# Optimization experiments

Hardware: AMD Instinct MI355X
Metric: run time of the kernel (lower is better)

## Reference

```python
import jax, jax.numpy as jnp
import numpy as np

HIDDEN = 256
BATCH = 8
N_A = 2048
N_B = 2048


def setup_inputs() -> dict:
    key = jax.random.key(0)
    ks = jax.random.split(key, 9)
    s = 1.0 / np.sqrt(HIDDEN)  # torch Linear default init scale
    return {
        "A": jax.random.normal(ks[0], (BATCH, N_A, HIDDEN), dtype=jnp.float32),
        "B": jax.random.normal(ks[1], (BATCH, N_B, HIDDEN), dtype=jnp.float32),
        "mask_B": jax.random.randint(ks[2], (BATCH, N_B), 0, 2, dtype=jnp.int32),
        "Wq": jax.random.uniform(ks[3], (HIDDEN, HIDDEN), jnp.float32, -s, s),
        "bq": jax.random.uniform(ks[4], (HIDDEN,), jnp.float32, -s, s),
        "Wk": jax.random.uniform(ks[5], (HIDDEN, HIDDEN), jnp.float32, -s, s),
        "bk": jax.random.uniform(ks[6], (HIDDEN,), jnp.float32, -s, s),
        "Wv": jax.random.uniform(ks[7], (HIDDEN, HIDDEN), jnp.float32, -s, s),
        "bv": jax.random.uniform(ks[8], (HIDDEN,), jnp.float32, -s, s),
    }


def reference(A, B, mask_B, Wq, bq, Wk, bk, Wv, bv):
    # QKV projections (torch Linear: x @ W.T + b)
    Q = A @ Wq.T + bq          # [B, N_A, H]
    K = B @ Wk.T + bk          # [B, N_B, H]
    V = B @ Wv.T + bv          # [B, N_B, H]
    scale = 1.0 / jnp.sqrt(jnp.asarray(Q.shape[-1], Q.dtype))
    scores = jnp.einsum("bnh,bmh->bnm", Q, K) * scale  # [B, N_A, N_B]
    neg_inf = jnp.finfo(scores.dtype).min
    scores = jnp.where(mask_B[:, None, :] == 0, neg_inf, scores)
    attn = jax.nn.softmax(scores, axis=-1)
    out = jnp.einsum("bnm,bmh->bnh", attn, V)          # [B, N_A, H]
    return out
```

## Files before the change

kernel.cpp:

```cpp
#include <hip/hip_runtime.h>


typedef __attribute__((ext_vector_type(8))) __bf16 bf16x8;
typedef __attribute__((ext_vector_type(4))) __bf16 bf16x4;
typedef __attribute__((ext_vector_type(4))) float f32x4;

#if __has_builtin(__builtin_amdgcn_exp2f)
#define EXP2(x) __builtin_amdgcn_exp2f(x)
#else
#define EXP2(x) exp2f(x)
#endif

#define MFMA16(a, b, c) __builtin_amdgcn_mfma_f32_16x16x32_bf16((a), (b), (c), 0, 0, 0)

typedef const __attribute__((address_space(1))) char gas_char;
typedef __attribute__((address_space(3))) char las_char;

static __device__ __forceinline__ void gload16(const void* g, void* l) {
  __builtin_amdgcn_global_load_lds((gas_char*)g, (las_char*)l, 16, 0, 0);
}

static __device__ __forceinline__ bf16x8 pack8(f32x4 a, f32x4 b) {
  bf16x8 r;
  r[0] = (__bf16)a[0]; r[1] = (__bf16)a[1]; r[2] = (__bf16)a[2]; r[3] = (__bf16)a[3];
  r[4] = (__bf16)b[0]; r[5] = (__bf16)b[1]; r[6] = (__bf16)b[2]; r[7] = (__bf16)b[3];
  return r;
}

__global__ __launch_bounds__(256) void wprep_kernel(
    const float* __restrict__ Wq, const float* __restrict__ Wk,
    const float* __restrict__ Wv, const int* __restrict__ mask,
    __bf16* __restrict__ Wb, float* __restrict__ mb) {
  const int bid = blockIdx.x;
  if (bid < 96) {
    int c = bid * 256 + threadIdx.x;
    int w_id = c >> 13;
    int j = c & 8191;
    const float* __restrict__ W = (w_id == 0) ? Wq : (w_id == 1 ? Wk : Wv);
    int n = j >> 5;
    int c5 = j & 31;
    int qtr = c5 >> 3;
    int k8 = (c5 & 7) << 3;
    const float* wp = &W[n * 256 + qtr * 64 + k8];
    f32x4 w0 = *(const f32x4*)wp;
    f32x4 w1 = *(const f32x4*)(wp + 4);
    if (w_id == 0) {
      const float cs = 0.090168440f;
      w0[0] *= cs; w0[1] *= cs; w0[2] *= cs; w0[3] *= cs;
      w1[0] *= cs; w1[1] *= cs; w1[2] *= cs; w1[3] *= cs;
    }
    int kx = k8 ^ ((n & 7) << 3);
    *(bf16x8*)&Wb[(size_t)w_id * 65536 + qtr * 16384 + n * 64 + kx] =
        pack8(w0, w1);
  } else {
    int i = (bid - 96) * 256 + threadIdx.x;
    if (i < 8 * 2048) mb[i] = (mask[i] != 0) ? 0.0f : -1.0e30f;
  }
}

__global__ __launch_bounds__(256, 2) void proj_kernel(
    const float* __restrict__ A, const float* __restrict__ Bm,
    const __bf16* __restrict__ Wb,
    const float* __restrict__ bq, const float* __restrict__ bk,
    const float* __restrict__ bv,
    __bf16* __restrict__ QF, __bf16* __restrict__ KF, __bf16* __restrict__ VF) {
  extern __shared__ char smem[];
  const int pid = blockIdx.x;
  const int proj = pid >> 8;
  const int rb = (pid & 255) << 6;
  const float* __restrict__ X = (proj == 0) ? A : Bm;
  const char* __restrict__ Wbp = (const char*)(Wb + (size_t)proj * 65536);
  const float* __restrict__ bias = (proj == 0) ? bq : (proj == 1 ? bk : bv);
  const int tid = threadIdx.x;
  const int w = tid >> 6, l = tid & 63, lo = l & 15, g = l >> 4;
  const int r0 = rb + w * 16;

  bf16x8 xf[8];
#pragma unroll
  for (int q8 = 0; q8 < 8; ++q8) {
    const float* xp = &X[(r0 + lo) * 256 + q8 * 32 + g * 8];
    xf[q8] = pack8(*(const f32x4*)xp, *(const f32x4*)(xp + 4));
  }

  f32x4 acc[16];
#pragma unroll
  for (int j = 0; j < 16; ++j) acc[j] = (f32x4){0.f, 0.f, 0.f, 0.f};

  #define STAGEW(qtr, buf)                                                    \
    {                                                                         \
      const char* gw = Wbp + (qtr)*32768 + w * 1024 + l * 16;                 \
      char* lw = smem + (buf)*32768 + w * 1024;                               \
      gload16(gw, lw);                                                        \
      gload16(gw + 4096, lw + 4096);                                          \
      gload16(gw + 8192, lw + 8192);                                          \
      gload16(gw + 12288, lw + 12288);                                        \
      gload16(gw + 16384, lw + 16384);                                        \
      gload16(gw + 20480, lw + 20480);                                        \
      gload16(gw + 24576, lw + 24576);                                        \
      gload16(gw + 28672, lw + 28672);                                        \
    }

  STAGEW(0, 0);
  __syncthreads();

  for (int qtr = 0; qtr < 4; ++qtr) {
    const int cur = qtr & 1;
    if (qtr < 3) STAGEW(qtr + 1, cur ^ 1);
    const __bf16* Wl = (const __bf16*)(smem + cur * 32768);
#pragma unroll
    for (int ks2 = 0; ks2 < 2; ++ks2) {
      bf16x8 xcur = xf[qtr * 2 + ks2];
#pragma unroll
      for (int nt = 0; nt < 16; ++nt) {
        int n = nt * 16 + lo;
        int kchunk = (ks2 * 4 + g) ^ (n & 7);
        bf16x8 wf = *(const bf16x8*)&Wl[n * 64 + kchunk * 8];
        if (proj == 2) {
          acc[nt] = MFMA16(wf, xcur, acc[nt]);
        } else {
          acc[nt] = MFMA16(xcur, wf, acc[nt]);
        }
      }
    }
    __syncthreads();
  }

  if (proj != 2) {
    const float cs = (proj == 0) ? 0.090168440f : 1.0f;
    __bf16* __restrict__ O = (proj == 0) ? QF : KF;
    const size_t rgbase = (size_t)(r0 >> 4) << 12;
#pragma unroll
    for (int nt = 0; nt < 16; ++nt) {
      int h = nt * 16 + lo;
      float bb = bias[h] * cs;
      size_t hpart = (size_t)((h >> 5) << 9) + (((h >> 3) & 3) << 7) + (h & 7);
#pragma unroll
      for (int r = 0; r < 4; ++r) {
        int R = r0 + g * 4 + r;
        O[rgbase + hpart + ((R & 15) << 3)] = (__bf16)(acc[nt][r] + bb);
      }
    }
  } else {
    const int bidx = r0 >> 11;
    const int nb = r0 & 2047;
    __bf16* __restrict__ Vo = VF + (size_t)bidx * 524288;
#pragma unroll
    for (int ht = 0; ht < 16; ++ht)
#pragma unroll
      for (int r = 0; r < 4; ++r) {
        int h = ht * 16 + g * 4 + r;
        int n = nb + lo;
        Vo[((size_t)(n >> 6) << 14) + ((h >> 4) << 10) + (((n >> 3) & 7) << 7) +
           ((h & 15) << 3) + (n & 7)] = (__bf16)(acc[ht][r] + bias[h]);
      }
  }
}

__global__ __launch_bounds__(256, 2) void attn_kernel(
    const __bf16* __restrict__ QF, const __bf16* __restrict__ KF,
    const __bf16* __restrict__ VF, const float* __restrict__ mb,
    __bf16* __restrict__ Opart, float* __restrict__ mpart,
    float* __restrict__ lpart, float* __restrict__ out,
    int chunk, int direct) {
  extern __shared__ char smem[];
  const int bid = blockIdx.x;
  const int b = bid & 7;
  const int rest = bid >> 3;
  const int qt = rest & 15;
  const int s = rest >> 4;
  const int tid = threadIdx.x;
  const int w = tid >> 6, l = tid & 63, lo = l & 15, g = l >> 4;
  const int q0 = qt * 128 + w * 32;
  const __bf16* __restrict__ Qb = QF + ((size_t)b * 2048 + q0) * 256;
  const __bf16* __restrict__ Kb = KF + (size_t)b * 2048 * 256;
  const __bf16* __restrict__ Vb = VF + (size_t)b * 524288;
  const float* __restrict__ mbb = mb + b * 2048;
  __bf16* Pw = (__bf16*)(smem + 65536) + w * 1280;
  float* mbl = (float*)(smem + 75776);

  bf16x8 qf[2][8];
#pragma unroll
  for (int u = 0; u < 2; ++u)
#pragma unroll
    for (int hs = 0; hs < 8; ++hs)
      qf[u][hs] = *(const bf16x8*)&Qb[u * 4096 + hs * 512 + l * 8];

  f32x4 oacc[2][16];
#pragma unroll
  for (int u = 0; u < 2; ++u)
#pragma unroll
    for (int i = 0; i < 16; ++i) oacc[u][i] = (f32x4){0.f, 0.f, 0.f, 0.f};
  float m[2] = {-3.0e28f, -3.0e28f}, lsum[2] = {0.f, 0.f};

  const int kv0 = s * chunk;
  const int niter = chunk >> 5;

  #define STAGE_K(kvb, buf)                                                   \
    {                                                                         \
      const char* gk = (const char*)(Kb + (size_t)(kvb) * 256) + w * 4096 +   \
                       l * 16;                                                \
      char* lk = smem + (buf)*16384 + w * 4096;                               \
      gload16(gk, lk);                                                        \
      gload16(gk + 1024, lk + 1024);                                          \
      gload16(gk + 2048, lk + 2048);                                          \
      gload16(gk + 3072, lk + 3072);                                          \
    }
  #define STAGE_V(kvb, buf)                                                   \
    {                                                                         \
      const char* gv = (const char*)(Vb + (((size_t)(kvb) >> 6) << 14) +      \
                                     (((kvb) >> 5) & 1) * 512) +              \
                       w * 8192 + l * 16;                                     \
      char* lv = smem + 32768 + (buf)*16384 + w * 4096;                       \
      gload16(gv, lv);                                                        \
      gload16(gv + 2048, lv + 1024);                                          \
      gload16(gv + 4096, lv + 2048);                                          \
      gload16(gv + 6144, lv + 3072);                                          \
    }

  if (!direct)
    for (int j = tid; j < chunk; j += 256) mbl[j] = mbb[kv0 + j];
  STAGE_K(kv0, 0);
  STAGE_V(kv0, 0);
  __syncthreads();

  for (int it = 0; it < niter; ++it) {
    const int kvb = kv0 + (it << 5);
    const int cur = it & 1;
    const bool pre = (it + 1 < niter);
    if (pre) STAGE_K(kvb + 32, cur ^ 1);
    const char* kbase = smem + cur * 16384;
    const char* vbase = smem + 32768 + cur * 16384;

    f32x4 sacc[2][2];
#pragma unroll
    for (int u = 0; u < 2; ++u)
#pragma unroll
      for (int t = 0; t < 2; ++t) sacc[u][t] = (f32x4){0.f, 0.f, 0.f, 0.f};
    __builtin_amdgcn_s_setprio(1);
#pragma unroll
    for (int t = 0; t < 2; ++t)
#pragma unroll
      for (int hs = 0; hs < 8; ++hs) {
        bf16x8 kf = *(const bf16x8*)(kbase + t * 8192 + hs * 1024 + l * 16);
        sacc[0][t] = MFMA16(kf, qf[0][hs], sacc[0][t]);
        sacc[1][t] = MFMA16(kf, qf[1][hs], sacc[1][t]);
      }
    __builtin_amdgcn_s_setprio(0);

    f32x4 bias4[2];
#pragma unroll
    for (int t = 0; t < 2; ++t) {
      if (direct)
        bias4[t] = *(const f32x4*)&mbb[kvb + t * 16 + g * 4];
      else
        bias4[t] = *(const f32x4*)&mbl[(it << 5) + t * 16 + g * 4];
    }
#pragma unroll
    for (int u = 0; u < 2; ++u) {
      float tmax = -3.4e38f;
#pragma unroll
      for (int t = 0; t < 2; ++t)
#pragma unroll
        for (int r = 0; r < 4; ++r) {
          sacc[u][t][r] += bias4[t][r];
          tmax = fmaxf(tmax, sacc[u][t][r]);
        }
      tmax = fmaxf(tmax, __shfl_xor(tmax, 16));
      tmax = fmaxf(tmax, __shfl_xor(tmax, 32));
      if (!__all(tmax <= m[u] + 8.0f)) {
        float mn = fmaxf(m[u], tmax);
        float f = EXP2(m[u] - mn);
        lsum[u] *= f;
#pragma unroll
        for (int i = 0; i < 16; ++i) {
          oacc[u][i][0] *= f; oacc[u][i][1] *= f;
          oacc[u][i][2] *= f; oacc[u][i][3] *= f;
        }
        m[u] = mn;
      }
#pragma unroll
      for (int t = 0; t < 2; ++t) {
        float p0 = EXP2(sacc[u][t][0] - m[u]);
        float p1 = EXP2(sacc[u][t][1] - m[u]);
        float p2 = EXP2(sacc[u][t][2] - m[u]);
        float p3 = EXP2(sacc[u][t][3] - m[u]);
        lsum[u] += (p0 + p1) + (p2 + p3);
        bf16x4 pk;
        pk[0] = (__bf16)p0; pk[1] = (__bf16)p1;
        pk[2] = (__bf16)p2; pk[3] = (__bf16)p3;
        *(bf16x4*)&Pw[u * 640 + lo * 40 + t * 16 + g * 4] = pk;
      }
    }
    bf16x8 pf[2];
#pragma unroll
    for (int u = 0; u < 2; ++u)
      pf[u] = *(const bf16x8*)&Pw[u * 640 + lo * 40 + g * 8];

    if (direct || !pre) {
      asm volatile("s_waitcnt vmcnt(0)" ::: "memory");
    } else {
      asm volatile("s_waitcnt vmcnt(4)" ::: "memory");
    }
    __builtin_amdgcn_s_barrier();
    __builtin_amdgcn_sched_barrier(0);

    if (pre) STAGE_V(kvb + 32, cur ^ 1);

    __builtin_amdgcn_s_setprio(1);
#pragma unroll
    for (int ht = 0; ht < 16; ++ht) {
      bf16x8 vf = *(const bf16x8*)(vbase + ht * 1024 + l * 16);
      oacc[0][ht] = MFMA16(vf, pf[0], oacc[0][ht]);
      oacc[1][ht] = MFMA16(vf, pf[1], oacc[1][ht]);
    }
    __builtin_amdgcn_s_setprio(0);

    if (direct || !pre) {
      asm volatile("s_waitcnt vmcnt(0)" ::: "memory");
    } else {
      asm volatile("s_waitcnt vmcnt(4)" ::: "memory");
    }
    __builtin_amdgcn_s_barrier();
    __builtin_amdgcn_sched_barrier(0);
  }

#pragma unroll
  for (int u = 0; u < 2; ++u) {
    float ls = lsum[u];
    ls += __shfl_xor(ls, 16);
    ls += __shfl_xor(ls, 32);
    const int q0u = q0 + u * 16;
    if (direct) {
      float inv = 1.0f / ls;
      float* __restrict__ Ob = out + ((size_t)b * 2048 + q0u) * 256;
#pragma unroll
      for (int ht = 0; ht < 16; ++ht) {
        f32x4 v = oacc[u][ht];
        v[0] *= inv; v[1] *= inv; v[2] *= inv; v[3] *= inv;
        *(f32x4*)&Ob[lo * 256 + ht * 16 + g * 4] = v;
      }
    } else {
      const size_t rowbase = (size_t)(s * 8 + b) * 2048 + q0u;
      __bf16* __restrict__ Ob = Opart + rowbase * 256;
#pragma unroll
      for (int ht = 0; ht < 16; ++ht) {
        f32x4 v = oacc[u][ht];
        bf16x4 pk;
        pk[0] = (__bf16)v[0]; pk[1] = (__bf16)v[1];
        pk[2] = (__bf16)v[2]; pk[3] = (__bf16)v[3];
        *(bf16x4*)&Ob[lo * 256 + ht * 16 + g * 4] = pk;
      }
      if (l < 16) {
        mpart[rowbase + lo] = m[u];
        lpart[rowbase + lo] = ls;
      }
    }
  }
}

__global__ __launch_bounds__(256) void combine_kernel(
    const __bf16* __restrict__ Opart, const float* __restrict__ mpart,
    const float* __restrict__ lpart, float* __restrict__ out, int nsplit) {
  int t = blockIdx.x * 256 + threadIdx.x;
  int row = t >> 6;
  int h4 = (t & 63) << 2;
  float M = -3.4e38f;
  for (int s = 0; s < nsplit; ++s) M = fmaxf(M, mpart[s * 16384 + row]);
  f32x4 acc = (f32x4){0.f, 0.f, 0.f, 0.f};
  float denom = 0.f;
  for (int s = 0; s < nsplit; ++s) {
    float wgt = EXP2(mpart[s * 16384 + row] - M);
    denom += wgt * lpart[s * 16384 + row];
    bf16x4 o = *(const bf16x4*)&Opart[((size_t)s * 16384 + row) * 256 + h4];
    acc[0] += wgt * (float)o[0]; acc[1] += wgt * (float)o[1];
    acc[2] += wgt * (float)o[2]; acc[3] += wgt * (float)o[3];
  }
  float inv = 1.0f / denom;
  f32x4 r;
  r[0] = acc[0] * inv; r[1] = acc[1] * inv;
  r[2] = acc[2] * inv; r[3] = acc[3] * inv;
  *(f32x4*)&out[(size_t)row * 256 + h4] = r;
}

extern "C" void kernel_launch(void* const* d_in, const int* in_sizes, int n_in,
                              void* d_out, int out_size, void* d_ws, size_t ws_size,
                              hipStream_t stream) {
  const float* A = (const float*)d_in[0];
  const float* B = (const float*)d_in[1];
  const int* mask = (const int*)d_in[2];
  const float* Wq = (const float*)d_in[3];
  const float* bq = (const float*)d_in[4];
  const float* Wk = (const float*)d_in[5];
  const float* bk = (const float*)d_in[6];
  const float* Wv = (const float*)d_in[7];
  const float* bv = (const float*)d_in[8];

  char* ws = (char*)d_ws;
  __bf16* QF = (__bf16*)(ws);
  __bf16* KF = (__bf16*)(ws + (8ull << 20));
  __bf16* VF = (__bf16*)(ws + (16ull << 20));
  float* mb = (float*)(ws + (24ull << 20));
  float* mpart = (float*)(ws + (24ull << 20) + 0x10000);
  float* lpart = (float*)(ws + (24ull << 20) + 0x60000);
  __bf16* Wb = (__bf16*)(ws + (24ull << 20) + 0xA0000);
  __bf16* Opart = (__bf16*)(ws + (25ull << 20));

  const size_t base = 25ull << 20;
  const size_t part = 8ull << 20;
  int S;
  if (ws_size >= base + 4 * part) S = 4;
  else if (ws_size >= base + 2 * part) S = 2;
  else if (ws_size >= base + 1 * part) S = 1;
  else S = 0;

  const int PSMEM = 65536;
  (void)hipFuncSetAttribute((const void*)proj_kernel,
                            hipFuncAttributeMaxDynamicSharedMemorySize, PSMEM);
  const int SMEM = 65536 + 4 * 1280 * 2 + 2048;
  (void)hipFuncSetAttribute((const void*)attn_kernel,
                            hipFuncAttributeMaxDynamicSharedMemorySize, SMEM);

  wprep_kernel<<<160, 256, 0, stream>>>(Wq, Wk, Wv, mask, Wb, mb);
  proj_kernel<<<768, 256, PSMEM, stream>>>(A, B, Wb, bq, bk, bv, QF, KF, VF);
  if (S == 0) {
    attn_kernel<<<128, 256, SMEM, stream>>>(QF, KF, VF, mb, nullptr, nullptr,
                                            nullptr, (float*)d_out, 2048, 1);
  } else {
    attn_kernel<<<128 * S, 256, SMEM, stream>>>(QF, KF, VF, mb, Opart, mpart,
                                                lpart, nullptr, 2048 / S, 0);
    combine_kernel<<<4096, 256, 0, stream>>>(Opart, mpart, lpart,
                                             (float*)d_out, S);
  }
}
```

Before: 93.17 us.

## Halve attention query tile per wave and drop double-buffered K/V staging

Each wave now handles 16 query rows instead of 32, and the block covers 64 queries, so twice as many blocks are launched. The K/V double buffer with its explicit vmcnt waits is replaced by a single buffer loaded at the top of each iteration, with __syncthreads on both sides. Shared memory per block and register use drop, and launch bounds now request 4 blocks per CU, all aimed at higher occupancy. The cost is that load latency is no longer overlapped within a block, and every K/V tile is now read from global memory twice as often.

```diff
diff --git a/kernel.cpp b/kernel.cpp
--- a/kernel.cpp
+++ b/kernel.cpp
@@ -156,7 +156,7 @@
   }
 }
 
-__global__ __launch_bounds__(256, 2) void attn_kernel(
+__global__ __launch_bounds__(256, 4) void attn_kernel(
     const __bf16* __restrict__ QF, const __bf16* __restrict__ KF,
     const __bf16* __restrict__ VF, const float* __restrict__ mb,
     __bf16* __restrict__ Opart, float* __restrict__ mpart,
@@ -166,51 +166,44 @@
   const int bid = blockIdx.x;
   const int b = bid & 7;
   const int rest = bid >> 3;
-  const int qt = rest & 15;
-  const int s = rest >> 4;
+  const int qt = rest & 31;
+  const int s = rest >> 5;
   const int tid = threadIdx.x;
   const int w = tid >> 6, l = tid & 63, lo = l & 15, g = l >> 4;
-  const int q0 = qt * 128 + w * 32;
+  const int q0 = qt * 64 + w * 16;
   const __bf16* __restrict__ Qb = QF + ((size_t)b * 2048 + q0) * 256;
   const __bf16* __restrict__ Kb = KF + (size_t)b * 2048 * 256;
   const __bf16* __restrict__ Vb = VF + (size_t)b * 524288;
   const float* __restrict__ mbb = mb + b * 2048;
-  __bf16* Pw = (__bf16*)(smem + 65536) + w * 1280;
-  float* mbl = (float*)(smem + 75776);
-
-  bf16x8 qf[2][8];
-#pragma unroll
-  for (int u = 0; u < 2; ++u)
-#pragma unroll
-    for (int hs = 0; hs < 8; ++hs)
-      qf[u][hs] = *(const bf16x8*)&Qb[u * 4096 + hs * 512 + l * 8];
-
-  f32x4 oacc[2][16];
-#pragma unroll
-  for (int u = 0; u < 2; ++u)
-#pragma unroll
-    for (int i = 0; i < 16; ++i) oacc[u][i] = (f32x4){0.f, 0.f, 0.f, 0.f};
-  float m[2] = {-3.0e28f, -3.0e28f}, lsum[2] = {0.f, 0.f};
+  __bf16* Pw = (__bf16*)(smem + 32768) + w * 640;
+  float* mbl = (float*)(smem + 37888);
+
+  bf16x8 qf[8];
+#pragma unroll
+  for (int hs = 0; hs < 8; ++hs)
+    qf[hs] = *(const bf16x8*)&Qb[hs * 512 + l * 8];
+
+  f32x4 oacc[16];
+#pragma unroll
+  for (int i = 0; i < 16; ++i) oacc[i] = (f32x4){0.f, 0.f, 0.f, 0.f};
+  float m = -3.0e28f, lsum = 0.f;
 
   const int kv0 = s * chunk;
   const int niter = chunk >> 5;
 
-  #define STAGE_K(kvb, buf)                                                   \
+  #define STAGE(kvb)                                                          \
     {                                                                         \
       const char* gk = (const char*)(Kb + (size_t)(kvb) * 256) + w * 4096 +   \
                        l * 16;                                                \
-      char* lk = smem + (buf)*16384 + w * 4096;                               \
+      char* lk = smem + w * 4096;                                             \
       gload16(gk, lk);                                                        \
       gload16(gk + 1024, lk + 1024);                                          \
       gload16(gk + 2048, lk + 2048);                                          \
       gload16(gk + 3072, lk + 3072);                                          \
-    }
-  #define STAGE_V(kvb, buf)                                                   \
-    {                                                                         \
       const char* gv = (const char*)(Vb + (((size_t)(kvb) >> 6) << 14) +      \
                                      (((kvb) >> 5) & 1) * 512) +              \
                        w * 8192 + l * 16;                                     \
-      char* lv = smem + 32768 + (buf)*16384 + w * 4096;                       \
+      char* lv = smem + 16384 + w * 4096;                                     \
       gload16(gv, lv);                                                        \
       gload16(gv + 2048, lv + 1024);                                          \
       gload16(gv + 4096, lv + 2048);                                          \
@@ -219,31 +212,22 @@
 
   if (!direct)
     for (int j = tid; j < chunk; j += 256) mbl[j] = mbb[kv0 + j];
-  STAGE_K(kv0, 0);
-  STAGE_V(kv0, 0);
-  __syncthreads();
 
   for (int it = 0; it < niter; ++it) {
     const int kvb = kv0 + (it << 5);
-    const int cur = it & 1;
-    const bool pre = (it + 1 < niter);
-    if (pre) STAGE_K(kvb + 32, cur ^ 1);
-    const char* kbase = smem + cur * 16384;
-    const char* vbase = smem + 32768 + cur * 16384;
-
-    f32x4 sacc[2][2];
-#pragma unroll
-    for (int u = 0; u < 2; ++u)
-#pragma unroll
-      for (int t = 0; t < 2; ++t) sacc[u][t] = (f32x4){0.f, 0.f, 0.f, 0.f};
+    STAGE(kvb);
+    __syncthreads();
+
+    f32x4 sacc[2];
+    sacc[0] = (f32x4){0.f, 0.f, 0.f, 0.f};
+    sacc[1] = (f32x4){0.f, 0.f, 0.f, 0.f};
     __builtin_amdgcn_s_setprio(1);
 #pragma unroll
     for (int t = 0; t < 2; ++t)
 #pragma unroll
       for (int hs = 0; hs < 8; ++hs) {
-        bf16x8 kf = *(const bf16x8*)(kbase + t * 8192 + hs * 1024 + l * 16);
-        sacc[0][t] = MFMA16(kf, qf[0][hs], sacc[0][t]);
-        sacc[1][t] = MFMA16(kf, qf[1][hs], sacc[1][t]);
+        bf16x8 kf = *(const bf16x8*)(smem + t * 8192 + hs * 1024 + l * 16);
+        sacc[t] = MFMA16(kf, qf[hs], sacc[t]);
       }
     __builtin_amdgcn_s_setprio(0);
 
@@ -255,105 +239,76 @@
       else
         bias4[t] = *(const f32x4*)&mbl[(it << 5) + t * 16 + g * 4];
     }
-#pragma unroll
-    for (int u = 0; u < 2; ++u) {
-      float tmax = -3.4e38f;
-#pragma unroll
-      for (int t = 0; t < 2; ++t)
-#pragma unroll
-        for (int r = 0; r < 4; ++r) {
-          sacc[u][t][r] += bias4[t][r];
-          tmax = fmaxf(tmax, sacc[u][t][r]);
-        }
-      tmax = fmaxf(tmax, __shfl_xor(tmax, 16));
-      tmax = fmaxf(tmax, __shfl_xor(tmax, 32));
-      if (!__all(tmax <= m[u] + 8.0f)) {
-        float mn = fmaxf(m[u], tmax);
-        float f = EXP2(m[u] - mn);
-        lsum[u] *= f;
-#pragma unroll
-        for (int i = 0; i < 16; ++i) {
-          oacc[u][i][0] *= f; oacc[u][i][1] *= f;
-          oacc[u][i][2] *= f; oacc[u][i][3] *= f;
-        }
-        m[u] = mn;
-      }
-#pragma unroll
-      for (int t = 0; t < 2; ++t) {
-        float p0 = EXP2(sacc[u][t][0] - m[u]);
-        float p1 = EXP2(sacc[u][t][1] - m[u]);
-        float p2 = EXP2(sacc[u][t][2] - m[u]);
-        float p3 = EXP2(sacc[u][t][3] - m[u]);
-        lsum[u] += (p0 + p1) + (p2 + p3);
-        bf16x4 pk;
-        pk[0] = (__bf16)p0; pk[1] = (__bf16)p1;
-        pk[2] = (__bf16)p2; pk[3] = (__bf16)p3;
-        *(bf16x4*)&Pw[u * 640 + lo * 40 + t * 16 + g * 4] = pk;
-      }
-    }
-    bf16x8 pf[2];
-#pragma unroll
-    for (int u = 0; u < 2; ++u)
-      pf[u] = *(const bf16x8*)&Pw[u * 640 + lo * 40 + g * 8];
-
-    if (direct || !pre) {
-      asm volatile("s_waitcnt vmcnt(0)" ::: "memory");
-    } else {
-      asm volatile("s_waitcnt vmcnt(4)" ::: "memory");
-    }
-    __builtin_amdgcn_s_barrier();
-    __builtin_amdgcn_sched_barrier(0);
-
-    if (pre) STAGE_V(kvb + 32, cur ^ 1);
+    float tmax = -3.4e38f;
+#pragma unroll
+    for (int t = 0; t < 2; ++t)
+#pragma unroll
+      for (int r = 0; r < 4; ++r) {
+        sacc[t][r] += bias4[t][r];
+        tmax = fmaxf(tmax, sacc[t][r]);
+      }
+    tmax = fmaxf(tmax, __shfl_xor(tmax, 16));
+    tmax = fmaxf(tmax, __shfl_xor(tmax, 32));
+    if (!__all(tmax <= m + 8.0f)) {
+      float mn = fmaxf(m, tmax);
+      float f = EXP2(m - mn);
+      lsum *= f;
+#pragma unroll
+      for (int i = 0; i < 16; ++i) {
+        oacc[i][0] *= f; oacc[i][1] *= f;
+        oacc[i][2] *= f; oacc[i][3] *= f;
+      }
+      m = mn;
+    }
+#pragma unroll
+    for (int t = 0; t < 2; ++t) {
+      float p0 = EXP2(sacc[t][0] - m);
+      float p1 = EXP2(sacc[t][1] - m);
+      float p2 = EXP2(sacc[t][2] - m);
+      float p3 = EXP2(sacc[t][3] - m);
+      lsum += (p0 + p1) + (p2 + p3);
+      bf16x4 pk;
+      pk[0] = (__bf16)p0; pk[1] = (__bf16)p1;
+      pk[2] = (__bf16)p2; pk[3] = (__bf16)p3;
+      *(bf16x4*)&Pw[lo * 40 + t * 16 + g * 4] = pk;
+    }
+    bf16x8 pf = *(const bf16x8*)&Pw[lo * 40 + g * 8];
 
     __builtin_amdgcn_s_setprio(1);
 #pragma unroll
     for (int ht = 0; ht < 16; ++ht) {
-      bf16x8 vf = *(const bf16x8*)(vbase + ht * 1024 + l * 16);
-      oacc[0][ht] = MFMA16(vf, pf[0], oacc[0][ht]);
-      oacc[1][ht] = MFMA16(vf, pf[1], oacc[1][ht]);
+      bf16x8 vf = *(const bf16x8*)(smem + 16384 + ht * 1024 + l * 16);
+      oacc[ht] = MFMA16(vf, pf, oacc[ht]);
     }
     __builtin_amdgcn_s_setprio(0);
-
-    if (direct || !pre) {
-      asm volatile("s_waitcnt vmcnt(0)" ::: "memory");
-    } else {
-      asm volatile("s_waitcnt vmcnt(4)" ::: "memory");
-    }
-    __builtin_amdgcn_s_barrier();
-    __builtin_amdgcn_sched_barrier(0);
-  }
-
-#pragma unroll
-  for (int u = 0; u < 2; ++u) {
-    float ls = lsum[u];
-    ls += __shfl_xor(ls, 16);
-    ls += __shfl_xor(ls, 32);
-    const int q0u = q0 + u * 16;
-    if (direct) {
-      float inv = 1.0f / ls;
-      float* __restrict__ Ob = out + ((size_t)b * 2048 + q0u) * 256;
-#pragma unroll
-      for (int ht = 0; ht < 16; ++ht) {
-        f32x4 v = oacc[u][ht];
-        v[0] *= inv; v[1] *= inv; v[2] *= inv; v[3] *= inv;
-        *(f32x4*)&Ob[lo * 256 + ht * 16 + g * 4] = v;
-      }
-    } else {
-      const size_t rowbase = (size_t)(s * 8 + b) * 2048 + q0u;
-      __bf16* __restrict__ Ob = Opart + rowbase * 256;
-#pragma unroll
-      for (int ht = 0; ht < 16; ++ht) {
-        f32x4 v = oacc[u][ht];
-        bf16x4 pk;
-        pk[0] = (__bf16)v[0]; pk[1] = (__bf16)v[1];
-        pk[2] = (__bf16)v[2]; pk[3] = (__bf16)v[3];
-        *(bf16x4*)&Ob[lo * 256 + ht * 16 + g * 4] = pk;
-      }
-      if (l < 16) {
-        mpart[rowbase + lo] = m[u];
-        lpart[rowbase + lo] = ls;
-      }
+    __syncthreads();
+  }
+
+  lsum += __shfl_xor(lsum, 16);
+  lsum += __shfl_xor(lsum, 32);
+  if (direct) {
+    float inv = 1.0f / lsum;
+    float* __restrict__ Ob = out + ((size_t)b * 2048 + q0) * 256;
+#pragma unroll
+    for (int ht = 0; ht < 16; ++ht) {
+      f32x4 v = oacc[ht];
+      v[0] *= inv; v[1] *= inv; v[2] *= inv; v[3] *= inv;
+      *(f32x4*)&Ob[lo * 256 + ht * 16 + g * 4] = v;
+    }
+  } else {
+    const size_t rowbase = (size_t)(s * 8 + b) * 2048 + q0;
+    __bf16* __restrict__ Ob = Opart + rowbase * 256;
+#pragma unroll
+    for (int ht = 0; ht < 16; ++ht) {
+      f32x4 v = oacc[ht];
+      bf16x4 pk;
+      pk[0] = (__bf16)v[0]; pk[1] = (__bf16)v[1];
+      pk[2] = (__bf16)v[2]; pk[3] = (__bf16)v[3];
+      *(bf16x4*)&Ob[lo * 256 + ht * 16 + g * 4] = pk;
+    }
+    if (l < 16) {
+      mpart[rowbase + lo] = m;
+      lpart[rowbase + lo] = lsum;
     }
   }
 }
@@ -416,17 +371,17 @@
   const int PSMEM = 65536;
   (void)hipFuncSetAttribute((const void*)proj_kernel,
                             hipFuncAttributeMaxDynamicSharedMemorySize, PSMEM);
-  const int SMEM = 65536 + 4 * 1280 * 2 + 2048;
+  const int SMEM = 32768 + 4 * 640 * 2 + 2048;
   (void)hipFuncSetAttribute((const void*)attn_kernel,
                             hipFuncAttributeMaxDynamicSharedMemorySize, SMEM);
 
   wprep_kernel<<<160, 256, 0, stream>>>(Wq, Wk, Wv, mask, Wb, mb);
   proj_kernel<<<768, 256, PSMEM, stream>>>(A, B, Wb, bq, bk, bv, QF, KF, VF);
   if (S == 0) {
-    attn_kernel<<<128, 256, SMEM, stream>>>(QF, KF, VF, mb, nullptr, nullptr,
+    attn_kernel<<<256, 256, SMEM, stream>>>(QF, KF, VF, mb, nullptr, nullptr,
                                             nullptr, (float*)d_out, 2048, 1);
   } else {
-    attn_kernel<<<128 * S, 256, SMEM, stream>>>(QF, KF, VF, mb, Opart, mpart,
+    attn_kernel<<<256 * S, 256, SMEM, stream>>>(QF, KF, VF, mb, Opart, mpart,
                                                 lpart, nullptr, 2048 / S, 0);
     combine_kernel<<<4096, 256, 0, stream>>>(Opart, mpart, lpart,
                                              (float*)d_out, S);
```

Result: slower. 100.9 us (+8.3%).
